# Performance work log

Measured on AMD Instinct MI355X. Metric: run time of the kernel, lower is better.

The kernel has to match this reference:

```python
import jax, jax.numpy as jnp
import numpy as np


def setup_inputs() -> dict:
    key = jax.random.key(0)
    ks = jax.random.split(key, 8)
    B, Q, K, F, FV, C = 8, 2048, 2048, 512, 512, 2
    q = jax.random.normal(ks[0], (B, Q, F), dtype=jnp.float32)
    k = jax.random.normal(ks[1], (B, K, F), dtype=jnp.float32)
    v = jax.random.normal(ks[2], (B, K, FV), dtype=jnp.float32)
    coords_q = jax.random.uniform(ks[3], (B, Q, C), dtype=jnp.float32)
    coords_k = jax.random.uniform(ks[4], (B, K, C), dtype=jnp.float32)
    attn_mask = jax.random.randint(ks[5], (B, Q, K), 0, 2).astype(bool)
    alibi_mask = jax.random.randint(ks[6], (B, Q, K), 0, 2).astype(bool)
    bias_scale = jax.random.uniform(ks[7], (1,), dtype=jnp.float32)
    return {"q": q, "k": k, "v": v, "coords_q": coords_q, "coords_k": coords_k,
            "attn_mask": attn_mask, "alibi_mask": alibi_mask, "bias_scale": bias_scale}


def reference(q, k, v, coords_q, coords_k, attn_mask, alibi_mask, bias_scale):
    # scaled dot-product logits: [B, Q, K]
    scale = k.shape[-1] ** -0.5
    weight_logits = jnp.einsum('bqf,bkf->bqk', q, k) * scale
    # pairwise Euclidean coordinate distances: [B, Q, K]
    diff = coords_q[:, :, None, :] - coords_k[:, None, :, :]
    distances = jnp.linalg.norm(diff, axis=-1)
    # _RunningMeanScaler in eval mode divides by running_mean == 1 (identity)
    scaled_distances = distances * bias_scale  # bias_scale broadcasts from [1]
    scaled_distances = jnp.where(alibi_mask, 0.0, scaled_distances)
    weights = jax.nn.softmax(weight_logits, axis=-1)
    # post-softmax bias subtraction + masking (non-standard attention)
    weights = jnp.where(attn_mask, 0.0, weights - scaled_distances)
    attention = jnp.einsum('bqk,bkf->bqf', weights, v)
    return attention
```

## Files before the change

### kernel.cpp

```cpp
#include <hip/hip_runtime.h>
#include <hip/hip_bf16.h>
#include <math.h>

#define BN  8
#define QN  2048
#define KN  2048
#define FN  512
#define FVN 512

typedef __bf16 bf16x8 __attribute__((ext_vector_type(8)));
typedef __bf16 bf16x4v __attribute__((ext_vector_type(4)));
typedef float  f32x4  __attribute__((ext_vector_type(4)));

__device__ inline bf16x8 pack8(float4 a, float4 b) {
  bf16x8 r;
  r[0] = (__bf16)a.x; r[1] = (__bf16)a.y; r[2] = (__bf16)a.z; r[3] = (__bf16)a.w;
  r[4] = (__bf16)b.x; r[5] = (__bf16)b.y; r[6] = (__bf16)b.z; r[7] = (__bf16)b.w;
  return r;
}

__device__ __forceinline__ void g2l16(const __bf16* g, __bf16* l) {
  __builtin_amdgcn_global_load_lds(
      (const __attribute__((address_space(1))) void*)g,
      (__attribute__((address_space(3))) void*)l,
      16, 0, 0);
}

__global__ __launch_bounds__(256) void prep(
    const float* __restrict__ qm, const float* __restrict__ km,
    const float* __restrict__ vm,
    __bf16* __restrict__ qb, __bf16* __restrict__ kb, __bf16* __restrict__ Vt,
    float* __restrict__ sums) {
  const int tid = threadIdx.x;
  if (blockIdx.y == 0) {
    const size_t idx = ((size_t)blockIdx.x * 256 + tid) * 8;
    const float scale = 0.044194173824159216f;
    float4 a = *(const float4*)(qm + idx);
    float4 b = *(const float4*)(qm + idx + 4);
    a.x *= scale; a.y *= scale; a.z *= scale; a.w *= scale;
    b.x *= scale; b.y *= scale; b.z *= scale; b.w *= scale;
    *(bf16x8*)(qb + idx) = pack8(a, b);
  } else if (blockIdx.y == 1) {
    const size_t idx = ((size_t)blockIdx.x * 256 + tid) * 8;
    float4 a = *(const float4*)(km + idx);
    float4 b = *(const float4*)(km + idx + 4);
    *(bf16x8*)(kb + idx) = pack8(a, b);
  } else if (blockIdx.y == 2) {
    const int bx = blockIdx.x;
    if (bx >= (KN / 64) * (FVN / 64) * BN) return;
    const int b  = bx >> 8;
    const int f0 = ((bx >> 5) & 7) * 64;
    const int k0 = (bx & 31) * 64;
    __shared__ float tile[64][65];
    const int r = tid >> 4;
    const int c = (tid & 15) * 4;
#pragma unroll
    for (int i = 0; i < 4; i++) {
      float4 u = *(const float4*)(vm + ((size_t)b * KN + k0 + r + i * 16) * FVN + f0 + c);
      tile[r + i * 16][c] = u.x; tile[r + i * 16][c + 1] = u.y;
      tile[r + i * 16][c + 2] = u.z; tile[r + i * 16][c + 3] = u.w;
    }
    __syncthreads();
#pragma unroll
    for (int i = 0; i < 4; i++) {
      int fv = r + i * 16;
      bf16x4v w;
      w[0] = (__bf16)tile[c][fv];     w[1] = (__bf16)tile[c + 1][fv];
      w[2] = (__bf16)tile[c + 2][fv]; w[3] = (__bf16)tile[c + 3][fv];
      *(bf16x4v*)(Vt + ((size_t)b * FVN + f0 + fv) * KN + k0 + c) = w;
    }
  } else {
    if (blockIdx.x < (BN * QN) / 1024) {
      float4 z4; z4.x = 0.f; z4.y = 0.f; z4.z = 0.f; z4.w = 0.f;
      ((float4*)sums)[(size_t)blockIdx.x * 256 + tid] = z4;
    }
  }
}

__global__ __launch_bounds__(256) void gemm_s(
    const __bf16* __restrict__ qb, const __bf16* __restrict__ kb,
    __bf16* __restrict__ Sws, float* __restrict__ sums,
    int b0, int q0, int qchunk) {
  __shared__ __align__(16) __bf16 As[2][128][32];
  __shared__ __align__(16) __bf16 Bs[2][128][32];
  const int tid = threadIdx.x;
  const int lane = tid & 63, wave = tid >> 6;
  const int wq = (wave & 1) * 64, wk = (wave >> 1) * 64;
  const int qt = blockIdx.x * 128, kt = blockIdx.y * 128;
  const int z = blockIdx.z, b = b0 + z;
  __bf16* S = Sws + (size_t)z * qchunk * KN;
  const __bf16* Ab = qb + ((size_t)b * QN + q0 + qt) * FN;
  const __bf16* Bb = kb + ((size_t)b * KN + kt) * FN;
  const int srow = lane >> 2;
  const int scol = (lane & 3) * 8;
  const int r = lane & 15, quad = lane >> 4;
  f32x4 acc[4][4] = {};
  for (int f0 = 0; f0 < FN; f0 += 64) {
    __syncthreads();
#pragma unroll
    for (int h = 0; h < 2; h++) {
      const int co = f0 + h * 32 + scol;
      g2l16(Ab + (size_t)(wave * 32 + srow) * FN + co,      &As[h][wave * 32][0]);
      g2l16(Ab + (size_t)(wave * 32 + 16 + srow) * FN + co, &As[h][wave * 32 + 16][0]);
      g2l16(Bb + (size_t)(wave * 32 + srow) * FN + co,      &Bs[h][wave * 32][0]);
      g2l16(Bb + (size_t)(wave * 32 + 16 + srow) * FN + co, &Bs[h][wave * 32 + 16][0]);
    }
    __syncthreads();
#pragma unroll
    for (int h = 0; h < 2; h++) {
      bf16x8 af[4], bf[4];
#pragma unroll
      for (int i = 0; i < 4; i++) af[i] = *(bf16x8*)&As[h][wq + i * 16 + r][quad * 8];
#pragma unroll
      for (int j = 0; j < 4; j++) bf[j] = *(bf16x8*)&Bs[h][wk + j * 16 + r][quad * 8];
#pragma unroll
      for (int i = 0; i < 4; i++)
#pragma unroll
        for (int j = 0; j < 4; j++)
          acc[i][j] = __builtin_amdgcn_mfma_f32_16x16x32_bf16(af[i], bf[j], acc[i][j], 0, 0, 0);
    }
  }
#pragma unroll
  for (int i = 0; i < 4; i++)
#pragma unroll
    for (int j = 0; j < 4; j++)
#pragma unroll
      for (int t = 0; t < 4; t++) {
        int qq = qt + wq + i * 16 + quad * 4 + t;
        int kk = kt + wk + j * 16 + r;
        S[(size_t)qq * KN + kk] = (__bf16)acc[i][j][t];
      }
#pragma unroll
  for (int i = 0; i < 4; i++)
#pragma unroll
    for (int t = 0; t < 4; t++) {
      float part = 0.f;
#pragma unroll
      for (int j = 0; j < 4; j++) part += __expf(acc[i][j][t]);
      part += __shfl_xor(part, 1);
      part += __shfl_xor(part, 2);
      part += __shfl_xor(part, 4);
      part += __shfl_xor(part, 8);
      if (r == 0)
        atomicAdd(&sums[(size_t)b * QN + q0 + qt + wq + i * 16 + quad * 4 + t], part);
    }
}

__global__ __launch_bounds__(256) void softmax_w(
    __bf16* __restrict__ Sws,
    const float* __restrict__ cq, const float* __restrict__ ck,
    const int* __restrict__ attn, const int* __restrict__ alibi,
    const float* __restrict__ bsp, const float* __restrict__ sums,
    int b0, int q0, int qchunk) {
  __shared__ float ckx[KN], cky[KN];
  const int z = blockIdx.z, b = b0 + z;
  const int lane = threadIdx.x & 63, wave = threadIdx.x >> 6;
  const int ql = blockIdx.x * 4 + wave;
  const int qg = q0 + ql;
  __bf16* Srow = Sws + ((size_t)z * qchunk + ql) * KN;
  const int* arow = attn + ((size_t)b * QN + qg) * KN;
  const int* lrow = alibi + ((size_t)b * QN + qg) * KN;
  const float* ckb = ck + (size_t)b * KN * 2;
  bf16x8 s8[4]; int4 am[8], al[8];
#pragma unroll
  for (int c = 0; c < 4; c++) {
    const int k0 = c * 512 + lane * 8;
    s8[c]       = *(const bf16x8*)(Srow + k0);
    am[c * 2]     = *(const int4*)(arow + k0);
    am[c * 2 + 1] = *(const int4*)(arow + k0 + 4);
    al[c * 2]     = *(const int4*)(lrow + k0);
    al[c * 2 + 1] = *(const int4*)(lrow + k0 + 4);
  }
  const float inv = 1.0f / sums[(size_t)b * QN + qg];
  const float qx = cq[((size_t)b * QN + qg) * 2 + 0];
  const float qy = cq[((size_t)b * QN + qg) * 2 + 1];
  const float bs = bsp[0];
  for (int i = threadIdx.x; i < KN / 2; i += 256) {
    float4 u = *(const float4*)(ckb + (size_t)i * 4);
    ckx[2 * i] = u.x;     cky[2 * i] = u.y;
    ckx[2 * i + 1] = u.z; cky[2 * i + 1] = u.w;
  }
  __syncthreads();
#pragma unroll
  for (int c = 0; c < 4; c++) {
    const int k0 = c * 512 + lane * 8;
    float4 x0 = *(const float4*)&ckx[k0]; float4 x1 = *(const float4*)&ckx[k0 + 4];
    float4 y0 = *(const float4*)&cky[k0]; float4 y1 = *(const float4*)&cky[k0 + 4];
    float kx[8] = {x0.x, x0.y, x0.z, x0.w, x1.x, x1.y, x1.z, x1.w};
    float ky[8] = {y0.x, y0.y, y0.z, y0.w, y1.x, y1.y, y1.z, y1.w};
    int amv[8] = {am[c * 2].x, am[c * 2].y, am[c * 2].z, am[c * 2].w,
                  am[c * 2 + 1].x, am[c * 2 + 1].y, am[c * 2 + 1].z, am[c * 2 + 1].w};
    int alv[8] = {al[c * 2].x, al[c * 2].y, al[c * 2].z, al[c * 2].w,
                  al[c * 2 + 1].x, al[c * 2 + 1].y, al[c * 2 + 1].z, al[c * 2 + 1].w};
    bf16x8 w8;
#pragma unroll
    for (int j = 0; j < 8; j++) {
      float p = __expf((float)s8[c][j]) * inv;
      float dx = qx - kx[j], dy = qy - ky[j];
      float sd = alv[j] ? 0.f : sqrtf(dx * dx + dy * dy) * bs;
      w8[j] = (__bf16)(amv[j] ? 0.f : (p - sd));
    }
    *(bf16x8*)(Srow + k0) = w8;
  }
}

__global__ __launch_bounds__(256) void gemm_w(
    const __bf16* __restrict__ W, const __bf16* __restrict__ Vt,
    float* __restrict__ out, int b0, int q0, int qchunk) {
  __shared__ __align__(16) __bf16 As[2][128][32];
  __shared__ __align__(16) __bf16 Bs[2][128][32];
  const int tid = threadIdx.x;
  const int lane = tid & 63, wave = tid >> 6;
  const int wq = (wave & 1) * 64, wf = (wave >> 1) * 64;
  const int qt = blockIdx.x * 128, ft = blockIdx.y * 128;
  const int z = blockIdx.z, b = b0 + z;
  const __bf16* Ab = W + ((size_t)z * qchunk + qt) * KN;
  const __bf16* Bb = Vt + ((size_t)b * FVN + ft) * KN;
  const int srow = lane >> 2;
  const int scol = (lane & 3) * 8;
  const int r = lane & 15, quad = lane >> 4;
  f32x4 acc[4][4] = {};
  for (int k0 = 0; k0 < KN; k0 += 64) {
    __syncthreads();
#pragma unroll
    for (int h = 0; h < 2; h++) {
      const int co = k0 + h * 32 + scol;
      g2l16(Ab + (size_t)(wave * 32 + srow) * KN + co,      &As[h][wave * 32][0]);
      g2l16(Ab + (size_t)(wave * 32 + 16 + srow) * KN + co, &As[h][wave * 32 + 16][0]);
      g2l16(Bb + (size_t)(wave * 32 + srow) * KN + co,      &Bs[h][wave * 32][0]);
      g2l16(Bb + (size_t)(wave * 32 + 16 + srow) * KN + co, &Bs[h][wave * 32 + 16][0]);
    }
    __syncthreads();
#pragma unroll
    for (int h = 0; h < 2; h++) {
      bf16x8 af[4], bf[4];
#pragma unroll
      for (int i = 0; i < 4; i++) af[i] = *(bf16x8*)&As[h][wq + i * 16 + r][quad * 8];
#pragma unroll
      for (int j = 0; j < 4; j++) bf[j] = *(bf16x8*)&Bs[h][wf + j * 16 + r][quad * 8];
#pragma unroll
      for (int i = 0; i < 4; i++)
#pragma unroll
        for (int j = 0; j < 4; j++)
          acc[i][j] = __builtin_amdgcn_mfma_f32_16x16x32_bf16(af[i], bf[j], acc[i][j], 0, 0, 0);
    }
  }
#pragma unroll
  for (int i = 0; i < 4; i++)
#pragma unroll
    for (int j = 0; j < 4; j++)
#pragma unroll
      for (int t = 0; t < 4; t++) {
        int qq = q0 + qt + wq + i * 16 + quad * 4 + t;
        int fv = ft + wf + j * 16 + r;
        out[((size_t)b * QN + qq) * FVN + fv] = acc[i][j][t];
      }
}

extern "C" void kernel_launch(void* const* d_in, const int* in_sizes, int n_in,
                              void* d_out, int out_size, void* d_ws, size_t ws_size,
                              hipStream_t stream) {
  (void)in_sizes; (void)n_in; (void)out_size;
  const float* qm   = (const float*)d_in[0];
  const float* km   = (const float*)d_in[1];
  const float* vm   = (const float*)d_in[2];
  const float* cq   = (const float*)d_in[3];
  const float* ck   = (const float*)d_in[4];
  const int*   attn = (const int*)d_in[5];
  const int*   alibi= (const int*)d_in[6];
  const float* bsp  = (const float*)d_in[7];
  float* out = (float*)d_out;

  __bf16* qb  = (__bf16*)d_ws;
  __bf16* kb  = qb + (size_t)BN * QN * FN;
  __bf16* Vt  = kb + (size_t)BN * KN * FN;
  float*  sums = (float*)(Vt + (size_t)BN * FVN * KN);
  __bf16* Sws = (__bf16*)(sums + (size_t)BN * QN);
  const size_t fixed = ((size_t)BN * QN * FN + (size_t)BN * KN * FN +
                        (size_t)BN * FVN * KN) * 2 + (size_t)BN * QN * 4;
  int nb = BN, qc = QN;
  while (nb > 1 && fixed + (size_t)nb * qc * KN * 2 > ws_size) nb >>= 1;
  while (qc > 128 && fixed + (size_t)nb * qc * KN * 2 > ws_size) qc >>= 1;

  prep<<<dim3((BN * QN * FN) / 2048, 4), 256, 0, stream>>>(qm, km, vm, qb, kb, Vt, sums);
  for (int b0 = 0; b0 < BN; b0 += nb) {
    for (int q0 = 0; q0 < QN; q0 += qc) {
      gemm_s<<<dim3(qc / 128, KN / 128, nb), 256, 0, stream>>>(qb, kb, Sws, sums, b0, q0, qc);
      softmax_w<<<dim3(qc / 4, 1, nb), 256, 0, stream>>>(Sws, cq, ck, attn, alibi, bsp,
                                                         sums, b0, q0, qc);
      gemm_w<<<dim3(qc / 128, FVN / 128, nb), 256, 0, stream>>>(Sws, Vt, out, b0, q0, qc);
    }
  }
}
```

Baseline: 481.4 us.

## Restructure softmax_w to one row per block with direct global-to-LDS loads

The elementwise softmax/bias kernel now gives each 256-thread block a single query row instead of four. The score row and both mask rows are staged into LDS with global_load_lds, and key coordinates are read straight from global memory into registers instead of being transposed through shared memory. This is meant to raise memory-level parallelism and reduce the per-block coordinate-staging overhead in this bandwidth-bound pass. In exchange it launches four times as many blocks, re-reads the key coordinates for every row, and uses narrower 4-element stores.

```diff
diff --git a/kernel.cpp b/kernel.cpp
--- a/kernel.cpp
+++ b/kernel.cpp
@@ -20,6 +20,12 @@
 }
 
 __device__ __forceinline__ void g2l16(const __bf16* g, __bf16* l) {
+  __builtin_amdgcn_global_load_lds(
+      (const __attribute__((address_space(1))) void*)g,
+      (__attribute__((address_space(3))) void*)l,
+      16, 0, 0);
+}
+__device__ __forceinline__ void g2l16v(const void* g, void* l) {
   __builtin_amdgcn_global_load_lds(
       (const __attribute__((address_space(1))) void*)g,
       (__attribute__((address_space(3))) void*)l,
@@ -152,55 +158,58 @@
     const int* __restrict__ attn, const int* __restrict__ alibi,
     const float* __restrict__ bsp, const float* __restrict__ sums,
     int b0, int q0, int qchunk) {
-  __shared__ float ckx[KN], cky[KN];
+  __shared__ __align__(16) __bf16 S_lds[KN];
+  __shared__ __align__(16) int    am_lds[KN];
+  __shared__ __align__(16) int    al_lds[KN];
+  const int tid = threadIdx.x;
+  const int lane = tid & 63, wave = tid >> 6;
   const int z = blockIdx.z, b = b0 + z;
-  const int lane = threadIdx.x & 63, wave = threadIdx.x >> 6;
-  const int ql = blockIdx.x * 4 + wave;
+  const int ql = blockIdx.x;
   const int qg = q0 + ql;
   __bf16* Srow = Sws + ((size_t)z * qchunk + ql) * KN;
   const int* arow = attn + ((size_t)b * QN + qg) * KN;
   const int* lrow = alibi + ((size_t)b * QN + qg) * KN;
   const float* ckb = ck + (size_t)b * KN * 2;
-  bf16x8 s8[4]; int4 am[8], al[8];
-#pragma unroll
-  for (int c = 0; c < 4; c++) {
-    const int k0 = c * 512 + lane * 8;
-    s8[c]       = *(const bf16x8*)(Srow + k0);
-    am[c * 2]     = *(const int4*)(arow + k0);
-    am[c * 2 + 1] = *(const int4*)(arow + k0 + 4);
-    al[c * 2]     = *(const int4*)(lrow + k0);
-    al[c * 2 + 1] = *(const int4*)(lrow + k0 + 4);
-  }
+  g2l16v((const char*)Srow + wave * 1024 + lane * 16,
+         (char*)S_lds + wave * 1024);
+#pragma unroll
+  for (int s = 0; s < 2; s++) {
+    const int seg = wave + s * 4;
+    g2l16v((const char*)arow + seg * 1024 + lane * 16, (char*)am_lds + seg * 1024);
+    g2l16v((const char*)lrow + seg * 1024 + lane * 16, (char*)al_lds + seg * 1024);
+  }
+  const int k0g = tid * 4;
+  const int k1g = 1024 + tid * 4;
+  float4 c00 = *(const float4*)(ckb + (size_t)k0g * 2);
+  float4 c01 = *(const float4*)(ckb + (size_t)k0g * 2 + 4);
+  float4 c10 = *(const float4*)(ckb + (size_t)k1g * 2);
+  float4 c11 = *(const float4*)(ckb + (size_t)k1g * 2 + 4);
   const float inv = 1.0f / sums[(size_t)b * QN + qg];
   const float qx = cq[((size_t)b * QN + qg) * 2 + 0];
   const float qy = cq[((size_t)b * QN + qg) * 2 + 1];
   const float bs = bsp[0];
-  for (int i = threadIdx.x; i < KN / 2; i += 256) {
-    float4 u = *(const float4*)(ckb + (size_t)i * 4);
-    ckx[2 * i] = u.x;     cky[2 * i] = u.y;
-    ckx[2 * i + 1] = u.z; cky[2 * i + 1] = u.w;
-  }
   __syncthreads();
 #pragma unroll
-  for (int c = 0; c < 4; c++) {
-    const int k0 = c * 512 + lane * 8;
-    float4 x0 = *(const float4*)&ckx[k0]; float4 x1 = *(const float4*)&ckx[k0 + 4];
-    float4 y0 = *(const float4*)&cky[k0]; float4 y1 = *(const float4*)&cky[k0 + 4];
-    float kx[8] = {x0.x, x0.y, x0.z, x0.w, x1.x, x1.y, x1.z, x1.w};
-    float ky[8] = {y0.x, y0.y, y0.z, y0.w, y1.x, y1.y, y1.z, y1.w};
-    int amv[8] = {am[c * 2].x, am[c * 2].y, am[c * 2].z, am[c * 2].w,
-                  am[c * 2 + 1].x, am[c * 2 + 1].y, am[c * 2 + 1].z, am[c * 2 + 1].w};
-    int alv[8] = {al[c * 2].x, al[c * 2].y, al[c * 2].z, al[c * 2].w,
-                  al[c * 2 + 1].x, al[c * 2 + 1].y, al[c * 2 + 1].z, al[c * 2 + 1].w};
-    bf16x8 w8;
-#pragma unroll
-    for (int j = 0; j < 8; j++) {
-      float p = __expf((float)s8[c][j]) * inv;
+  for (int g = 0; g < 2; g++) {
+    const int k = g ? k1g : k0g;
+    bf16x4v s4 = *(const bf16x4v*)((const char*)S_lds + (size_t)k * 2);
+    int4 am4 = *(const int4*)&am_lds[k];
+    int4 al4 = *(const int4*)&al_lds[k];
+    float4 ca = g ? c10 : c00;
+    float4 cb = g ? c11 : c01;
+    float kx[4] = {ca.x, ca.z, cb.x, cb.z};
+    float ky[4] = {ca.y, ca.w, cb.y, cb.w};
+    int amv[4] = {am4.x, am4.y, am4.z, am4.w};
+    int alv[4] = {al4.x, al4.y, al4.z, al4.w};
+    bf16x4v w4;
+#pragma unroll
+    for (int j = 0; j < 4; j++) {
+      float p = __expf((float)s4[j]) * inv;
       float dx = qx - kx[j], dy = qy - ky[j];
       float sd = alv[j] ? 0.f : sqrtf(dx * dx + dy * dy) * bs;
-      w8[j] = (__bf16)(amv[j] ? 0.f : (p - sd));
-    }
-    *(bf16x8*)(Srow + k0) = w8;
+      w4[j] = (__bf16)(amv[j] ? 0.f : (p - sd));
+    }
+    *(bf16x4v*)(Srow + k) = w4;
   }
 }
 
@@ -286,8 +295,8 @@
   for (int b0 = 0; b0 < BN; b0 += nb) {
     for (int q0 = 0; q0 < QN; q0 += qc) {
       gemm_s<<<dim3(qc / 128, KN / 128, nb), 256, 0, stream>>>(qb, kb, Sws, sums, b0, q0, qc);
-      softmax_w<<<dim3(qc / 4, 1, nb), 256, 0, stream>>>(Sws, cq, ck, attn, alibi, bsp,
-                                                         sums, b0, q0, qc);
+      softmax_w<<<dim3(qc, 1, nb), 256, 0, stream>>>(Sws, cq, ck, attn, alibi, bsp,
+                                                     sums, b0, q0, qc);
       gemm_w<<<dim3(qc / 128, FVN / 128, nb), 256, 0, stream>>>(Sws, Vt, out, b0, q0, qc);
     }
   }
```

Result: no change. 473.2 us (-1.7%).

## Fuse softmax/bias/mask weight computation into the P·V GEMM A-tile load

Applied to the files above, without the earlier changes.

Removes the separate softmax_w pass, which wrote bf16 weights back to the workspace. The new gemm_wf kernel reads raw logits plus the attn/alibi masks, builds the weight tile in registers and stores it straight into LDS as the GEMM A operand. The Q tile shrinks to 64 rows, and the next tile's logits and masks are prefetched while the MFMAs run. This saves one launch and one round trip of the weight matrix. The cost is that the int32 masks and the logits are re-read and the exp/sqrt work is recomputed by each of the 4 FV column blocks, and the smaller tile lowers operand reuse.

```diff
diff --git a/kernel.cpp b/kernel.cpp
--- a/kernel.cpp
+++ b/kernel.cpp
@@ -146,107 +146,122 @@
     }
 }
 
-__global__ __launch_bounds__(256) void softmax_w(
-    __bf16* __restrict__ Sws,
+__global__ __launch_bounds__(256) void gemm_wf(
+    const __bf16* __restrict__ Sws, const __bf16* __restrict__ Vt,
+    const float* __restrict__ sums,
     const float* __restrict__ cq, const float* __restrict__ ck,
     const int* __restrict__ attn, const int* __restrict__ alibi,
-    const float* __restrict__ bsp, const float* __restrict__ sums,
+    const float* __restrict__ bsp, float* __restrict__ out,
     int b0, int q0, int qchunk) {
+  __shared__ __align__(16) __bf16 As[2][64][32];
+  __shared__ __align__(16) __bf16 Bs[2][128][32];
   __shared__ float ckx[KN], cky[KN];
+  const int tid = threadIdx.x;
+  const int lane = tid & 63, wave = tid >> 6;
+  const int qt = blockIdx.x * 64, ft = blockIdx.y * 128;
   const int z = blockIdx.z, b = b0 + z;
-  const int lane = threadIdx.x & 63, wave = threadIdx.x >> 6;
-  const int ql = blockIdx.x * 4 + wave;
-  const int qg = q0 + ql;
-  __bf16* Srow = Sws + ((size_t)z * qchunk + ql) * KN;
-  const int* arow = attn + ((size_t)b * QN + qg) * KN;
-  const int* lrow = alibi + ((size_t)b * QN + qg) * KN;
-  const float* ckb = ck + (size_t)b * KN * 2;
-  bf16x8 s8[4]; int4 am[8], al[8];
-#pragma unroll
-  for (int c = 0; c < 4; c++) {
-    const int k0 = c * 512 + lane * 8;
-    s8[c]       = *(const bf16x8*)(Srow + k0);
-    am[c * 2]     = *(const int4*)(arow + k0);
-    am[c * 2 + 1] = *(const int4*)(arow + k0 + 4);
-    al[c * 2]     = *(const int4*)(lrow + k0);
-    al[c * 2 + 1] = *(const int4*)(lrow + k0 + 4);
-  }
+  const int arow_l = tid >> 2;
+  const int c4 = tid & 3;
+  const int qg = q0 + qt + arow_l;
+  const __bf16* Srow = Sws + ((size_t)z * qchunk + qt + arow_l) * KN;
+  const int* amrow = attn + ((size_t)b * QN + qg) * KN;
+  const int* alrow = alibi + ((size_t)b * QN + qg) * KN;
   const float inv = 1.0f / sums[(size_t)b * QN + qg];
   const float qx = cq[((size_t)b * QN + qg) * 2 + 0];
   const float qy = cq[((size_t)b * QN + qg) * 2 + 1];
   const float bs = bsp[0];
-  for (int i = threadIdx.x; i < KN / 2; i += 256) {
+  const int srow = lane >> 2, scol = (lane & 3) * 8;
+  const __bf16* Bb = Vt + ((size_t)b * FVN + ft) * KN;
+  const int r = lane & 15, quad = lane >> 4;
+  const int wq = (wave & 1) * 32, wf = (wave >> 1) * 64;
+  const float* ckb = ck + (size_t)b * KN * 2;
+  for (int i = tid; i < KN / 2; i += 256) {
     float4 u = *(const float4*)(ckb + (size_t)i * 4);
     ckx[2 * i] = u.x;     cky[2 * i] = u.y;
     ckx[2 * i + 1] = u.z; cky[2 * i + 1] = u.w;
   }
+  f32x4 acc[2][4] = {};
+  bf16x8 s8a, s8b; int4 amv[4], alv[4];
+  {
+    const int kk = c4 * 16;
+    s8a = *(const bf16x8*)(Srow + kk);
+    s8b = *(const bf16x8*)(Srow + kk + 8);
+#pragma unroll
+    for (int i = 0; i < 4; i++) {
+      amv[i] = *(const int4*)(amrow + kk + i * 4);
+      alv[i] = *(const int4*)(alrow + kk + i * 4);
+    }
+  }
   __syncthreads();
-#pragma unroll
-  for (int c = 0; c < 4; c++) {
-    const int k0 = c * 512 + lane * 8;
-    float4 x0 = *(const float4*)&ckx[k0]; float4 x1 = *(const float4*)&ckx[k0 + 4];
-    float4 y0 = *(const float4*)&cky[k0]; float4 y1 = *(const float4*)&cky[k0 + 4];
-    float kx[8] = {x0.x, x0.y, x0.z, x0.w, x1.x, x1.y, x1.z, x1.w};
-    float ky[8] = {y0.x, y0.y, y0.z, y0.w, y1.x, y1.y, y1.z, y1.w};
-    int amv[8] = {am[c * 2].x, am[c * 2].y, am[c * 2].z, am[c * 2].w,
-                  am[c * 2 + 1].x, am[c * 2 + 1].y, am[c * 2 + 1].z, am[c * 2 + 1].w};
-    int alv[8] = {al[c * 2].x, al[c * 2].y, al[c * 2].z, al[c * 2].w,
-                  al[c * 2 + 1].x, al[c * 2 + 1].y, al[c * 2 + 1].z, al[c * 2 + 1].w};
-    bf16x8 w8;
-#pragma unroll
-    for (int j = 0; j < 8; j++) {
-      float p = __expf((float)s8[c][j]) * inv;
-      float dx = qx - kx[j], dy = qy - ky[j];
-      float sd = alv[j] ? 0.f : sqrtf(dx * dx + dy * dy) * bs;
-      w8[j] = (__bf16)(amv[j] ? 0.f : (p - sd));
-    }
-    *(bf16x8*)(Srow + k0) = w8;
-  }
-}
-
-__global__ __launch_bounds__(256) void gemm_w(
-    const __bf16* __restrict__ W, const __bf16* __restrict__ Vt,
-    float* __restrict__ out, int b0, int q0, int qchunk) {
-  __shared__ __align__(16) __bf16 As[2][128][32];
-  __shared__ __align__(16) __bf16 Bs[2][128][32];
-  const int tid = threadIdx.x;
-  const int lane = tid & 63, wave = tid >> 6;
-  const int wq = (wave & 1) * 64, wf = (wave >> 1) * 64;
-  const int qt = blockIdx.x * 128, ft = blockIdx.y * 128;
-  const int z = blockIdx.z, b = b0 + z;
-  const __bf16* Ab = W + ((size_t)z * qchunk + qt) * KN;
-  const __bf16* Bb = Vt + ((size_t)b * FVN + ft) * KN;
-  const int srow = lane >> 2;
-  const int scol = (lane & 3) * 8;
-  const int r = lane & 15, quad = lane >> 4;
-  f32x4 acc[4][4] = {};
   for (int k0 = 0; k0 < KN; k0 += 64) {
-    __syncthreads();
+    {
+      const int kk = k0 + c4 * 16;
+      float kxv[16], kyv[16];
+#pragma unroll
+      for (int j4 = 0; j4 < 4; j4++) {
+        float4 x4 = *(const float4*)&ckx[kk + j4 * 4];
+        float4 y4 = *(const float4*)&cky[kk + j4 * 4];
+        kxv[j4 * 4 + 0] = x4.x; kxv[j4 * 4 + 1] = x4.y;
+        kxv[j4 * 4 + 2] = x4.z; kxv[j4 * 4 + 3] = x4.w;
+        kyv[j4 * 4 + 0] = y4.x; kyv[j4 * 4 + 1] = y4.y;
+        kyv[j4 * 4 + 2] = y4.z; kyv[j4 * 4 + 3] = y4.w;
+      }
+      int amA[16] = {amv[0].x, amv[0].y, amv[0].z, amv[0].w,
+                     amv[1].x, amv[1].y, amv[1].z, amv[1].w,
+                     amv[2].x, amv[2].y, amv[2].z, amv[2].w,
+                     amv[3].x, amv[3].y, amv[3].z, amv[3].w};
+      int alA[16] = {alv[0].x, alv[0].y, alv[0].z, alv[0].w,
+                     alv[1].x, alv[1].y, alv[1].z, alv[1].w,
+                     alv[2].x, alv[2].y, alv[2].z, alv[2].w,
+                     alv[3].x, alv[3].y, alv[3].z, alv[3].w};
+      bf16x8 w0, w1;
+#pragma unroll
+      for (int j = 0; j < 16; j++) {
+        float sv = (j < 8) ? (float)s8a[j] : (float)s8b[j - 8];
+        float p = __expf(sv) * inv;
+        float dx = qx - kxv[j], dy = qy - kyv[j];
+        float sd = alA[j] ? 0.f : sqrtf(dx * dx + dy * dy) * bs;
+        float w = amA[j] ? 0.f : (p - sd);
+        if (j < 8) w0[j] = (__bf16)w; else w1[j - 8] = (__bf16)w;
+      }
+      const int h = c4 >> 1, off = (c4 & 1) * 16;
+      *(bf16x8*)&As[h][arow_l][off]     = w0;
+      *(bf16x8*)&As[h][arow_l][off + 8] = w1;
+    }
 #pragma unroll
     for (int h = 0; h < 2; h++) {
       const int co = k0 + h * 32 + scol;
-      g2l16(Ab + (size_t)(wave * 32 + srow) * KN + co,      &As[h][wave * 32][0]);
-      g2l16(Ab + (size_t)(wave * 32 + 16 + srow) * KN + co, &As[h][wave * 32 + 16][0]);
       g2l16(Bb + (size_t)(wave * 32 + srow) * KN + co,      &Bs[h][wave * 32][0]);
       g2l16(Bb + (size_t)(wave * 32 + 16 + srow) * KN + co, &Bs[h][wave * 32 + 16][0]);
     }
     __syncthreads();
+    if (k0 + 64 < KN) {
+      const int kk = k0 + 64 + c4 * 16;
+      s8a = *(const bf16x8*)(Srow + kk);
+      s8b = *(const bf16x8*)(Srow + kk + 8);
+#pragma unroll
+      for (int i = 0; i < 4; i++) {
+        amv[i] = *(const int4*)(amrow + kk + i * 4);
+        alv[i] = *(const int4*)(alrow + kk + i * 4);
+      }
+    }
 #pragma unroll
     for (int h = 0; h < 2; h++) {
-      bf16x8 af[4], bf[4];
-#pragma unroll
-      for (int i = 0; i < 4; i++) af[i] = *(bf16x8*)&As[h][wq + i * 16 + r][quad * 8];
+      bf16x8 af[2], bf[4];
+#pragma unroll
+      for (int i = 0; i < 2; i++) af[i] = *(bf16x8*)&As[h][wq + i * 16 + r][quad * 8];
 #pragma unroll
       for (int j = 0; j < 4; j++) bf[j] = *(bf16x8*)&Bs[h][wf + j * 16 + r][quad * 8];
 #pragma unroll
-      for (int i = 0; i < 4; i++)
+      for (int i = 0; i < 2; i++)
 #pragma unroll
         for (int j = 0; j < 4; j++)
           acc[i][j] = __builtin_amdgcn_mfma_f32_16x16x32_bf16(af[i], bf[j], acc[i][j], 0, 0, 0);
     }
-  }
-#pragma unroll
-  for (int i = 0; i < 4; i++)
+    __syncthreads();
+  }
+#pragma unroll
+  for (int i = 0; i < 2; i++)
 #pragma unroll
     for (int j = 0; j < 4; j++)
 #pragma unroll
@@ -286,9 +301,9 @@
   for (int b0 = 0; b0 < BN; b0 += nb) {
     for (int q0 = 0; q0 < QN; q0 += qc) {
       gemm_s<<<dim3(qc / 128, KN / 128, nb), 256, 0, stream>>>(qb, kb, Sws, sums, b0, q0, qc);
-      softmax_w<<<dim3(qc / 4, 1, nb), 256, 0, stream>>>(Sws, cq, ck, attn, alibi, bsp,
-                                                         sums, b0, q0, qc);
-      gemm_w<<<dim3(qc / 128, FVN / 128, nb), 256, 0, stream>>>(Sws, Vt, out, b0, q0, qc);
-    }
-  }
-}
+      gemm_wf<<<dim3(qc / 64, FVN / 128, nb), 256, 0, stream>>>(Sws, Vt, sums, cq, ck,
+                                                                attn, alibi, bsp, out,
+                                                                b0, q0, qc);
+    }
+  }
+}
```

New measurement: 547.5 us. 13.7% more time.
